# Performance work log

Hardware: AMD Instinct MI355X
Metric: run time of the kernel (lower is better)

Reference implementation:

```python
import jax, jax.numpy as jnp
import numpy as np

T, B, I, Hd = 512, 64, 128, 1024
SIGMA = 0.01


def setup_inputs() -> dict:
    key = jax.random.key(0)
    k1, k2, k3 = jax.random.split(key, 3)
    X = jax.random.normal(k1, (T, B, I), dtype=jnp.float32)
    W_ih = jax.random.normal(k2, (I, Hd), dtype=jnp.float32) * SIGMA
    W_hh = jax.random.normal(k3, (Hd, Hd), dtype=jnp.float32) * SIGMA
    b_h = jnp.zeros((Hd,), dtype=jnp.float32)
    H0 = jnp.zeros((B, Hd), dtype=jnp.float32)
    return {"X": X, "W_ih": W_ih, "W_hh": W_hh, "b_h": b_h, "H0": H0}


def reference(X, W_ih, W_hh, b_h, H0):
    # Pre-batch the input projection across all timesteps (same math,
    # one big GEMM instead of T small ones): [T,B,I] @ [I,H] -> [T,B,H]
    Xp = jnp.einsum("tbi,ih->tbh", X, W_ih) + b_h

    def step(H, xp_t):
        H_new = jnp.tanh(xp_t + H @ W_hh)
        return H_new, H_new

    H_final, states = jax.lax.scan(step, H0, Xp)
    # states: [T, B, H] (stack of per-timestep hidden states), H_final: [B, H]
    return states, H_final
```

## Files before the change

### kernel.cpp

```cpp
#include <hip/hip_runtime.h>
#include <hip/hip_bf16.h>
#include <stdint.h>

#define T_STEPS 512
#define BATCH   64
#define IN_DIM  128
#define HID     1024
#define KTOT    (HID + IN_DIM)
#define NWAVES  4
#define THREADS (NWAVES * 64)

#define NGRP    4
#define NSL     16
#define NB      16
#define NKH     32
#define NKX     4
#define HBUF    32768
#define LDSB    73728

#define RING    16
#define DCLR    4
#define SLOT    (BATCH * HID)
#define SENT    0x7F7F7F7F

typedef float f32x4 __attribute__((ext_vector_type(4)));
typedef int   i32x4 __attribute__((ext_vector_type(4)));
typedef short s16x8 __attribute__((ext_vector_type(8)));
typedef uint32_t u32x2 __attribute__((ext_vector_type(2)));

#define MFMA16 __builtin_amdgcn_mfma_f32_16x16x32_bf16

__device__ __forceinline__ uint32_t cvt_pk_bf16(float a, float b) {
    uint32_t r;
    asm("v_cvt_pk_bf16_f32 %0, %1, %2" : "=v"(r) : "v"(a), "v"(b));
    return r;
}

union frag_u { uint32_t u[4]; s16x8 s; };

__device__ __forceinline__ s16x8 pack_bf16x8(f32x4 a, f32x4 b) {
    frag_u f;
    f.u[0] = cvt_pk_bf16(a.x, a.y);
    f.u[1] = cvt_pk_bf16(a.z, a.w);
    f.u[2] = cvt_pk_bf16(b.x, b.y);
    f.u[3] = cvt_pk_bf16(b.z, b.w);
    return f.s;
}

__device__ __forceinline__ uint16_t f32_to_bf16(float v) {
    uint32_t u = __builtin_bit_cast(uint32_t, v);
    return (uint16_t)((u + 0x7FFFu + ((u >> 16) & 1u)) >> 16);
}

__device__ __forceinline__ float tanh_fast(float x) {
    float e = __expf(2.0f * x);
    return 1.0f - 2.0f * __builtin_amdgcn_rcpf(e + 1.0f);
}

__device__ __forceinline__ int imax(int a, int b) { return a > b ? a : b; }
__device__ __forceinline__ int max4(f32x4 v) {
    i32x4 a = __builtin_bit_cast(i32x4, v);
    return imax(imax(a.x, a.y), imax(a.z, a.w));
}

__global__ void rnn_init_kernel(const float* __restrict__ H0,
                                uint16_t* __restrict__ comm) {
    int i = blockIdx.x * 256 + threadIdx.x;
    for (int e = i; e < SLOT; e += 64 * 256)
        comm[e] = f32_to_bf16(H0[e]);
}

__global__ __launch_bounds__(THREADS, 1)
void rnn_seq_kernel(const float* __restrict__ X, const float* __restrict__ Wih,
                    const float* __restrict__ Whh, const float* __restrict__ bh,
                    float* __restrict__ out, uint16_t* __restrict__ comm)
{
    extern __shared__ char lds[];

    const int tid = threadIdx.x;
    const int grp = blockIdx.x >> 4;
    const int p   = blockIdx.x & 15;
    const int lane = tid & 63, wv = tid >> 6;
    const int cb = lane & 15, kg = lane >> 4;
    const int hc0 = p * 64;
    const int b   = grp * NB + cb;

    s16x8 wreg[36];
    #pragma unroll
    for (int half = 0; half < 2; ++half) {
        for (int e = tid; e < 32 * KTOT; e += THREADS) {
            int c2 = e & 31;
            int k  = e >> 5;
            int hcol = hc0 + half * 32 + c2;
            float w = (k < HID) ? Whh[(size_t)k * HID + hcol]
                                : Wih[(size_t)(k - HID) * HID + hcol];
            uint32_t off = ((uint32_t)((c2 >> 4) * 36 + (k >> 5)) << 10)
                         + (((k >> 3) & 3) << 8) + ((c2 & 15) << 4) + ((k & 7) << 1);
            *(uint16_t*)(lds + off) = f32_to_bf16(w);
        }
        __syncthreads();
        if ((wv >> 1) == half) {
            const char* base = lds + (size_t)(wv & 1) * 36 * 1024 + lane * 16;
            #pragma unroll
            for (int kk = 0; kk < 36; ++kk)
                wreg[kk] = *(const s16x8*)(base + (size_t)kk * 1024);
        }
        __syncthreads();
    }

    const int h = hc0 + wv * 16 + kg * 4;
    const f32x4 bv = *(const f32x4*)(bh + h);

    uint16_t* wb = comm + (size_t)b * HID + h;
    float* ob = out + (size_t)b * HID + h;

    const size_t ssrc = (size_t)(grp * NB + (tid & 15)) * HID
                      + ((tid >> 4) & 3) * 8 + (tid >> 6) * 32;

    u32x2 sentv; sentv.x = SENT; sentv.y = SENT;

    for (int t = 0; t < T_STEPS; ++t) {
        f32x4 acc0 = {0.f,0.f,0.f,0.f}, acc1 = {0.f,0.f,0.f,0.f};

        const float* xrow = X + ((size_t)t * BATCH + b) * IN_DIM;
        #pragma unroll
        for (int kk = 0; kk < NKX; ++kk) {
            int kidx = kk * 32 + kg * 8;
            f32x4 f0 = *(const f32x4*)(xrow + kidx);
            f32x4 f1 = *(const f32x4*)(xrow + kidx + 4);
            s16x8 xf = pack_bf16x8(f0, f1);
            if (kk & 1) acc1 = MFMA16(wreg[32 + kk], xf, acc1, 0, 0, 0);
            else        acc0 = MFMA16(wreg[32 + kk], xf, acc0, 0, 0, 0);
        }
        __builtin_amdgcn_sched_barrier(0);

        char* Hb = lds + (size_t)(t & 1) * HBUF;
        const char* gsrc = (const char*)(comm + (size_t)(t & (RING - 1)) * SLOT
                                         + ssrc);
        f32x4 L[8];
        for (;;) {
            #pragma unroll
            for (int i = 0; i < 8; ++i)
                asm volatile("global_load_dwordx4 %0, %1, off sc0 sc1"
                             : "=v"(L[i]) : "v"(gsrc + (size_t)i * 256) : "memory");
            asm volatile("s_waitcnt vmcnt(0)" ::: "memory");
            __builtin_amdgcn_sched_barrier(0);
            int m = (int)0x80000000;
            #pragma unroll
            for (int i = 0; i < 8; ++i) m = imax(m, max4(L[i]));
            if (__all(m != (int)SENT)) break;
        }
        #pragma unroll
        for (int i = 0; i < 8; ++i)
            *(f32x4*)(Hb + tid * 16 + i * 4096) = L[i];
        __syncthreads();

        const char* hfb = Hb + lane * 16;
        #pragma unroll
        for (int kk = 0; kk < NKH; ++kk) {
            s16x8 af = *(const s16x8*)(hfb + (size_t)kk * 1024);
            if (kk & 1) acc1 = MFMA16(wreg[kk], af, acc1, 0, 0, 0);
            else        acc0 = MFMA16(wreg[kk], af, acc0, 0, 0, 0);
        }

        float t0 = tanh_fast(acc0[0] + acc1[0] + bv.x);
        float t1 = tanh_fast(acc0[1] + acc1[1] + bv.y);
        float t2 = tanh_fast(acc0[2] + acc1[2] + bv.z);
        float t3 = tanh_fast(acc0[3] + acc1[3] + bv.w);

        u32x2 cd;
        cd.x = cvt_pk_bf16(t0, t1);
        cd.y = cvt_pk_bf16(t2, t3);
        uint16_t* pw = wb + (size_t)((t + 1) & (RING - 1)) * SLOT;
        asm volatile("global_store_dwordx2 %0, %1, off sc0 sc1"
                     :: "v"(pw), "v"(cd) : "memory");
        {
            uint16_t* pc = wb + (size_t)((t + 1 + DCLR) & (RING - 1)) * SLOT;
            asm volatile("global_store_dwordx2 %0, %1, off sc0 sc1"
                         :: "v"(pc), "v"(sentv) : "memory");
        }

        f32x4 vo; vo.x = t0; vo.y = t1; vo.z = t2; vo.w = t3;
        *(f32x4*)(ob + (size_t)t * BATCH * HID) = vo;
        if (t == T_STEPS - 1)
            *(f32x4*)(ob + (size_t)T_STEPS * BATCH * HID) = vo;
    }
}

extern "C" void kernel_launch(void* const* d_in, const int* in_sizes, int n_in,
                              void* d_out, int out_size, void* d_ws, size_t ws_size,
                              hipStream_t stream) {
    (void)in_sizes; (void)n_in; (void)out_size; (void)ws_size;
    const float* X   = (const float*)d_in[0];
    const float* Wih = (const float*)d_in[1];
    const float* Whh = (const float*)d_in[2];
    const float* bh  = (const float*)d_in[3];
    const float* H0  = (const float*)d_in[4];
    float* out = (float*)d_out;

    uint16_t* comm = (uint16_t*)d_ws;

    hipFuncSetAttribute((const void*)rnn_seq_kernel,
                        hipFuncAttributeMaxDynamicSharedMemorySize, LDSB);

    hipMemsetAsync(comm, 0x7F, (size_t)RING * SLOT * 2, stream);
    hipLaunchKernelGGL(rnn_init_kernel, dim3(64), dim3(256), 0, stream, H0, comm);
    hipLaunchKernelGGL(rnn_seq_kernel, dim3(NGRP * NSL), dim3(THREADS), LDSB, stream,
                       X, Wih, Whh, bh, out, comm);
}
```

Before: 1.741 ms.

## Double-buffer spin-poll loads and widen MFMA accumulator chains to four

The spin-wait on the global ring buffer now keeps two batches of eight loads in flight and checks one while the other is pending. This aims to cut the round-trip latency of each poll when waiting for the previous step's hidden state. The sentinel clear store moves ahead of the barrier so it leaves the critical path after the tanh. The MFMA reduction uses four independent accumulators instead of two, giving shorter dependency chains and earlier LDS loads, at the cost of extra VGPRs and extra memory traffic from redundant polls.

```diff
diff --git a/kernel.cpp b/kernel.cpp
--- a/kernel.cpp
+++ b/kernel.cpp
@@ -62,6 +62,26 @@
     i32x4 a = __builtin_bit_cast(i32x4, v);
     return imax(imax(a.x, a.y), imax(a.z, a.w));
 }
+
+#define ISSUE8(D, P)                                                    \
+    asm volatile(                                                       \
+        "global_load_dwordx4 %0, %8, off sc0 sc1\n\t"                   \
+        "global_load_dwordx4 %1, %8, off offset:256 sc0 sc1\n\t"        \
+        "global_load_dwordx4 %2, %8, off offset:512 sc0 sc1\n\t"        \
+        "global_load_dwordx4 %3, %8, off offset:768 sc0 sc1\n\t"        \
+        "global_load_dwordx4 %4, %8, off offset:1024 sc0 sc1\n\t"       \
+        "global_load_dwordx4 %5, %8, off offset:1280 sc0 sc1\n\t"       \
+        "global_load_dwordx4 %6, %8, off offset:1536 sc0 sc1\n\t"       \
+        "global_load_dwordx4 %7, %8, off offset:1792 sc0 sc1"           \
+        : "=&v"(D[0]), "=&v"(D[1]), "=&v"(D[2]), "=&v"(D[3]),           \
+          "=&v"(D[4]), "=&v"(D[5]), "=&v"(D[6]), "=&v"(D[7])            \
+        : "v"(P)                                                        \
+        : "memory")
+
+#define SCAN8(D, M)                                                     \
+    { M = (int)0x80000000;                                              \
+      _Pragma("unroll")                                                 \
+      for (int _i = 0; _i < 8; ++_i) M = imax(M, max4(D[_i])); }
 
 __global__ void rnn_init_kernel(const float* __restrict__ H0,
                                 uint16_t* __restrict__ comm) {
@@ -120,53 +140,83 @@
     u32x2 sentv; sentv.x = SENT; sentv.y = SENT;
 
     for (int t = 0; t < T_STEPS; ++t) {
-        f32x4 acc0 = {0.f,0.f,0.f,0.f}, acc1 = {0.f,0.f,0.f,0.f};
+        f32x4 ac0 = {0.f,0.f,0.f,0.f}, ac1 = {0.f,0.f,0.f,0.f};
+        f32x4 ac2 = {0.f,0.f,0.f,0.f}, ac3 = {0.f,0.f,0.f,0.f};
 
         const float* xrow = X + ((size_t)t * BATCH + b) * IN_DIM;
-        #pragma unroll
-        for (int kk = 0; kk < NKX; ++kk) {
-            int kidx = kk * 32 + kg * 8;
-            f32x4 f0 = *(const f32x4*)(xrow + kidx);
-            f32x4 f1 = *(const f32x4*)(xrow + kidx + 4);
-            s16x8 xf = pack_bf16x8(f0, f1);
-            if (kk & 1) acc1 = MFMA16(wreg[32 + kk], xf, acc1, 0, 0, 0);
-            else        acc0 = MFMA16(wreg[32 + kk], xf, acc0, 0, 0, 0);
+        {
+            f32x4 f0 = *(const f32x4*)(xrow + kg * 8);
+            f32x4 f1 = *(const f32x4*)(xrow + kg * 8 + 4);
+            ac0 = MFMA16(wreg[32], pack_bf16x8(f0, f1), ac0, 0, 0, 0);
+            f0 = *(const f32x4*)(xrow + 32 + kg * 8);
+            f1 = *(const f32x4*)(xrow + 32 + kg * 8 + 4);
+            ac1 = MFMA16(wreg[33], pack_bf16x8(f0, f1), ac1, 0, 0, 0);
+            f0 = *(const f32x4*)(xrow + 64 + kg * 8);
+            f1 = *(const f32x4*)(xrow + 64 + kg * 8 + 4);
+            ac2 = MFMA16(wreg[34], pack_bf16x8(f0, f1), ac2, 0, 0, 0);
+            f0 = *(const f32x4*)(xrow + 96 + kg * 8);
+            f1 = *(const f32x4*)(xrow + 96 + kg * 8 + 4);
+            ac3 = MFMA16(wreg[35], pack_bf16x8(f0, f1), ac3, 0, 0, 0);
         }
         __builtin_amdgcn_sched_barrier(0);
 
         char* Hb = lds + (size_t)(t & 1) * HBUF;
         const char* gsrc = (const char*)(comm + (size_t)(t & (RING - 1)) * SLOT
                                          + ssrc);
-        f32x4 L[8];
+        f32x4 LA[8], LB[8];
+        asm volatile("s_waitcnt vmcnt(0)" ::: "memory");
+        __builtin_amdgcn_sched_barrier(0);
+        ISSUE8(LA, gsrc);
+        ISSUE8(LB, gsrc);
+        bool fromA;
         for (;;) {
+            asm volatile("s_waitcnt vmcnt(8)" ::: "memory");
+            __builtin_amdgcn_sched_barrier(0);
+            int m;
+            SCAN8(LA, m)
+            if (__all(m != (int)SENT)) { fromA = true; break; }
+            ISSUE8(LA, gsrc);
+            asm volatile("s_waitcnt vmcnt(8)" ::: "memory");
+            __builtin_amdgcn_sched_barrier(0);
+            SCAN8(LB, m)
+            if (__all(m != (int)SENT)) { fromA = false; break; }
+            ISSUE8(LB, gsrc);
+        }
+        asm volatile("s_waitcnt vmcnt(0)" ::: "memory");
+        __builtin_amdgcn_sched_barrier(0);
+        if (fromA) {
             #pragma unroll
             for (int i = 0; i < 8; ++i)
-                asm volatile("global_load_dwordx4 %0, %1, off sc0 sc1"
-                             : "=v"(L[i]) : "v"(gsrc + (size_t)i * 256) : "memory");
-            asm volatile("s_waitcnt vmcnt(0)" ::: "memory");
-            __builtin_amdgcn_sched_barrier(0);
-            int m = (int)0x80000000;
+                *(f32x4*)(Hb + tid * 16 + i * 4096) = LA[i];
+        } else {
             #pragma unroll
-            for (int i = 0; i < 8; ++i) m = imax(m, max4(L[i]));
-            if (__all(m != (int)SENT)) break;
-        }
-        #pragma unroll
-        for (int i = 0; i < 8; ++i)
-            *(f32x4*)(Hb + tid * 16 + i * 4096) = L[i];
+            for (int i = 0; i < 8; ++i)
+                *(f32x4*)(Hb + tid * 16 + i * 4096) = LB[i];
+        }
+        {
+            uint16_t* pc = wb + (size_t)((t + 1 + DCLR) & (RING - 1)) * SLOT;
+            asm volatile("global_store_dwordx2 %0, %1, off sc0 sc1"
+                         :: "v"(pc), "v"(sentv) : "memory");
+        }
         __syncthreads();
 
         const char* hfb = Hb + lane * 16;
         #pragma unroll
-        for (int kk = 0; kk < NKH; ++kk) {
-            s16x8 af = *(const s16x8*)(hfb + (size_t)kk * 1024);
-            if (kk & 1) acc1 = MFMA16(wreg[kk], af, acc1, 0, 0, 0);
-            else        acc0 = MFMA16(wreg[kk], af, acc0, 0, 0, 0);
-        }
-
-        float t0 = tanh_fast(acc0[0] + acc1[0] + bv.x);
-        float t1 = tanh_fast(acc0[1] + acc1[1] + bv.y);
-        float t2 = tanh_fast(acc0[2] + acc1[2] + bv.z);
-        float t3 = tanh_fast(acc0[3] + acc1[3] + bv.w);
+        for (int kk = 0; kk < NKH; kk += 4) {
+            s16x8 af0 = *(const s16x8*)(hfb + (size_t)(kk + 0) * 1024);
+            s16x8 af1 = *(const s16x8*)(hfb + (size_t)(kk + 1) * 1024);
+            s16x8 af2 = *(const s16x8*)(hfb + (size_t)(kk + 2) * 1024);
+            s16x8 af3 = *(const s16x8*)(hfb + (size_t)(kk + 3) * 1024);
+            ac0 = MFMA16(wreg[kk + 0], af0, ac0, 0, 0, 0);
+            ac1 = MFMA16(wreg[kk + 1], af1, ac1, 0, 0, 0);
+            ac2 = MFMA16(wreg[kk + 2], af2, ac2, 0, 0, 0);
+            ac3 = MFMA16(wreg[kk + 3], af3, ac3, 0, 0, 0);
+        }
+
+        float t0 = tanh_fast(ac0[0] + ac1[0] + ac2[0] + ac3[0] + bv.x);
+        float t1 = tanh_fast(ac0[1] + ac1[1] + ac2[1] + ac3[1] + bv.y);
+        float t2 = tanh_fast(ac0[2] + ac1[2] + ac2[2] + ac3[2] + bv.z);
+        float t3 = tanh_fast(ac0[3] + ac1[3] + ac2[3] + ac3[3] + bv.w);
 
         u32x2 cd;
         cd.x = cvt_pk_bf16(t0, t1);
@@ -174,11 +224,6 @@
         uint16_t* pw = wb + (size_t)((t + 1) & (RING - 1)) * SLOT;
         asm volatile("global_store_dwordx2 %0, %1, off sc0 sc1"
                      :: "v"(pw), "v"(cd) : "memory");
-        {
-            uint16_t* pc = wb + (size_t)((t + 1 + DCLR) & (RING - 1)) * SLOT;
-            asm volatile("global_store_dwordx2 %0, %1, off sc0 sc1"
-                         :: "v"(pc), "v"(sentv) : "memory");
-        }
 
         f32x4 vo; vo.x = t0; vo.y = t1; vo.z = t2; vo.w = t3;
         *(f32x4*)(ob + (size_t)t * BATCH * HID) = vo;
```

New measurement: 2.169 ms. 1.25x slower.
